# Kernel tuning notes

Hardware: AMD Instinct MI355X
Metric: run time of the kernel (lower is better)

The kernel has to match this reference:

```python
import jax, jax.numpy as jnp
import numpy as np

B, S, D, H = 4, 2048, 1024, 16
DH = D // H


def setup_inputs() -> dict:
    key = jax.random.key(0)
    k1, k2, k3 = jax.random.split(key, 3)
    x = jax.random.normal(k1, (B, S, D), dtype=jnp.float32)
    w_attn = jax.random.normal(k2, (D, 3 * D), dtype=jnp.float32) * 0.02
    b_attn = jnp.zeros((3 * D,), dtype=jnp.float32)
    w_proj = jax.random.normal(k3, (D, D), dtype=jnp.float32) * 0.02
    b_proj = jnp.zeros((D,), dtype=jnp.float32)
    return {"x": x, "w_attn": w_attn, "b_attn": b_attn, "w_proj": w_proj, "b_proj": b_proj}


def _split_heads(t):
    # [B, S, D] -> [B, H, S, DH]
    return t.reshape(B, S, H, DH).transpose(0, 2, 1, 3)


def reference(x, w_attn, b_attn, w_proj, b_proj):
    # fused QKV projection (TFConv1D = x @ w + b)
    qkv = jnp.einsum('bsd,df->bsf', x, w_attn) + b_attn  # [B, S, 3D]
    q, k, v = jnp.split(qkv, 3, axis=2)
    q, k, v = _split_heads(q), _split_heads(k), _split_heads(v)  # [B,H,S,DH]

    # scaled scores
    w = jnp.einsum('bhqd,bhkd->bhqk', q, k) / jnp.sqrt(jnp.asarray(DH, dtype=q.dtype))

    # causal mask: multiply + additive -10000 trick, as in original
    i = jnp.arange(S)[:, None]
    j = jnp.arange(S)[None, :]
    b = (i >= j).astype(w.dtype)  # nd == ns so i >= j - ns + nd == i >= j
    b = b[None, None]  # [1,1,S,S]
    w = w * b - 10000.0 * (1.0 - b)

    w = jax.nn.softmax(w, axis=-1)
    # attn_pdrop = 0.0 -> dropout is identity (eval)

    a = jnp.einsum('bhqk,bhkd->bhqd', w, v)  # [B,H,S,DH]
    a = a.transpose(0, 2, 1, 3).reshape(B, S, D)  # merge heads
    a = jnp.einsum('bsd,df->bsf', a, w_proj) + b_proj
    # resid_pdrop = 0.0 -> identity
    return a
```

## Files before the change

### kernel.cpp

```cpp
#include <hip/hip_runtime.h>
#include <stdint.h>

typedef __bf16 bf16x8 __attribute__((ext_vector_type(8)));
typedef float  f32x4  __attribute__((ext_vector_type(4)));

#define DEV __device__ __forceinline__

constexpr int Bc = 4, S = 2048, D = 1024, Hh = 16, DH = 64;
constexpr int Kdim = 1024;

DEV unsigned short f2bf(float f) {
    uint32_t u = __builtin_bit_cast(uint32_t, f);
    u += 0x7fff + ((u >> 16) & 1);
    return (unsigned short)(u >> 16);
}
DEV bf16x8 ld8(const unsigned short* p) {
    uint4 u = *(const uint4*)p;
    return __builtin_bit_cast(bf16x8, u);
}
DEV uint4 pack8(float4 a, float4 b) {
    union { uint4 u; unsigned short s[8]; } r;
    r.s[0] = f2bf(a.x); r.s[1] = f2bf(a.y); r.s[2] = f2bf(a.z); r.s[3] = f2bf(a.w);
    r.s[4] = f2bf(b.x); r.s[5] = f2bf(b.y); r.s[6] = f2bf(b.z); r.s[7] = f2bf(b.w);
    return r.u;
}

DEV void gl16(const void* g, void* l) {
    __builtin_amdgcn_global_load_lds((__attribute__((address_space(1))) void*)g,
                                     (__attribute__((address_space(3))) void*)l,
                                     16, 0, 0);
}

__global__ __launch_bounds__(256) void transpose_cvt(const float* __restrict__ in,
                                                     unsigned short* __restrict__ out,
                                                     int rows, int cols) {
    __shared__ float t[32][33];
    int tx = threadIdx.x & 31, ty = threadIdx.x >> 5;
    int c = blockIdx.x * 32 + tx;
    int rbase = blockIdx.y * 32;
    for (int rr = 0; rr < 32; rr += 8)
        t[ty + rr][tx] = in[(size_t)(rbase + ty + rr) * cols + c];
    __syncthreads();
    int orbase = blockIdx.x * 32;
    for (int rr = 0; rr < 32; rr += 8)
        out[(size_t)(orbase + ty + rr) * rows + rbase + tx] = f2bf(t[tx][ty + rr]);
}

__global__ __launch_bounds__(256) void cvt_bf16(const float* __restrict__ in,
                                                unsigned short* __restrict__ out) {
    size_t i = (size_t)blockIdx.x * 256 + threadIdx.x;
    const float4* p = (const float4*)(in + i * 8);
    float4 a = p[0], b = p[1];
    *(uint4*)(out + i * 8) = pack8(a, b);
}

__global__ __launch_bounds__(256) void gemm_bt(const unsigned short* __restrict__ A,
                                               const unsigned short* __restrict__ Bt,
                                               const float* __restrict__ bias,
                                               int mode,
                                               unsigned short* __restrict__ qo,
                                               unsigned short* __restrict__ ko,
                                               unsigned short* __restrict__ vo,
                                               float* __restrict__ outf) {
    __shared__ __align__(16) unsigned short As[2][128 * 64];
    __shared__ __align__(16) unsigned short Bs[2][128 * 64];
    const int tid = threadIdx.x;
    const int wave = tid >> 6, lane = tid & 63, g = lane >> 4, ln = lane & 15;
    const int wm = wave >> 1, wn = wave & 1;
    const int nwg = gridDim.x * gridDim.y;
    const int orig = blockIdx.y * gridDim.x + blockIdx.x;
    const int swz = (orig & 7) * (nwg >> 3) + (orig >> 3);
    const int m0 = (swz / gridDim.x) * 128, n0 = (swz % gridDim.x) * 128;

    f32x4 acc[4][4];
    for (int i = 0; i < 4; i++)
        for (int j = 0; j < 4; j++) acc[i][j] = f32x4{0.f, 0.f, 0.f, 0.f};

#define STAGE_G(buf, k0)                                                            \
    _Pragma("unroll")                                                               \
    for (int c = 0; c < 4; c++) {                                                   \
        int L = c * 4096 + tid * 16;                                                \
        int row = L >> 7;                                                           \
        int colb = (L & 127) ^ ((row & 7) << 4);                                    \
        gl16((const char*)A  + ((size_t)(m0 + row) * Kdim + (k0)) * 2 + colb,       \
             (char*)As[buf] + c * 4096 + wave * 1024);                              \
        gl16((const char*)Bt + ((size_t)(n0 + row) * Kdim + (k0)) * 2 + colb,       \
             (char*)Bs[buf] + c * 4096 + wave * 1024);                              \
    }

    STAGE_G(0, 0);
    asm volatile("s_waitcnt vmcnt(0)" ::: "memory");
    __builtin_amdgcn_s_barrier();
    asm volatile("" ::: "memory");

#pragma unroll 1
    for (int t = 0; t < 16; t++) {
        const int buf = t & 1;
        if (t + 1 < 16) STAGE_G(buf ^ 1, (t + 1) * 64);
        const unsigned short* Asb = As[buf];
        const unsigned short* Bsb = Bs[buf];
#pragma unroll
        for (int kk = 0; kk < 2; kk++) {
            bf16x8 af[4], bfr[4];
#pragma unroll
            for (int u = 0; u < 4; u++) {
                int ra = wm * 64 + u * 16 + ln;
                int rb = wn * 64 + u * 16 + ln;
                int co = kk * 64 + g * 16;
                af[u]  = ld8((const unsigned short*)((const char*)Asb + ra * 128 + (co ^ ((ra & 7) << 4))));
                bfr[u] = ld8((const unsigned short*)((const char*)Bsb + rb * 128 + (co ^ ((rb & 7) << 4))));
            }
#pragma unroll
            for (int mt = 0; mt < 4; mt++)
#pragma unroll
                for (int nt = 0; nt < 4; nt++)
                    acc[mt][nt] = __builtin_amdgcn_mfma_f32_16x16x32_bf16(af[mt], bfr[nt], acc[mt][nt], 0, 0, 0);
        }
        asm volatile("" ::: "memory");
        asm volatile("s_waitcnt vmcnt(0)" ::: "memory");
        __builtin_amdgcn_s_barrier();
        asm volatile("" ::: "memory");
    }
#undef STAGE_G

    for (int mt = 0; mt < 4; mt++)
        for (int nt = 0; nt < 4; nt++)
            for (int r = 0; r < 4; r++) {
                int m = m0 + wm * 64 + mt * 16 + g * 4 + r;
                int n = n0 + wn * 64 + nt * 16 + ln;
                float val = acc[mt][nt][r] + bias[n];
                if (mode == 0) {
                    int which = n >> 10, rem = n & 1023;
                    int hh = rem >> 6, dd = rem & 63;
                    int b = m >> 11, s = m & 2047;
                    int bh = (b << 4) + hh;
                    if (which == 0)      qo[((size_t)bh * S + s) * DH + dd] = f2bf(val);
                    else if (which == 1) ko[((size_t)bh * S + s) * DH + dd] = f2bf(val);
                    else                 vo[((size_t)bh * DH + dd) * S + s] = f2bf(val);
                } else {
                    outf[(size_t)m * 1024 + n] = val;
                }
            }
}

__global__ __launch_bounds__(512, 4) void attn_fwd(const unsigned short* __restrict__ qg,
                                                   const unsigned short* __restrict__ kg,
                                                   const unsigned short* __restrict__ vtg,
                                                   unsigned short* __restrict__ og) {
    __shared__ __align__(16) unsigned short Ks[128 * 64];
    __shared__ __align__(16) unsigned short Vs[64 * 128];
    __shared__ __align__(16) unsigned short P [128 * 136];
    const int idx = blockIdx.x;
    const int qt = 15 - (idx >> 6);
    const int bh = idx & 63;
    const int b = bh >> 4, h = bh & 15;
    const size_t base = (size_t)bh * S * DH;
    const unsigned short* qp = qg + base;
    const char* kpb  = (const char*)(kg  + base);
    const char* vtpb = (const char*)(vtg + base);
    const int tid = threadIdx.x, wave = tid >> 6, lane = tid & 63;
    const int g = lane >> 4, ln = lane & 15;
    const int q0 = qt * 128, wq = wave * 16;
    const int jn = qt + 1;

    bf16x8 qf[2];
    qf[0] = ld8(qp + (size_t)(q0 + wq + ln) * DH + g * 8);
    qf[1] = ld8(qp + (size_t)(q0 + wq + ln) * DH + 32 + g * 8);

    f32x4 o_t[4];
#pragma unroll
    for (int dt = 0; dt < 4; dt++) o_t[dt] = f32x4{0.f, 0.f, 0.f, 0.f};
    float m_ = -1e30f, l_ = 0.f;

#pragma unroll 1
    for (int j = 0; j < jn; j++) {
        const char* kj = kpb + (size_t)j * (128 * DH * 2);
        const char* vj = vtpb + j * 256;
#pragma unroll
        for (int c = 0; c < 2; c++) {
            int L = c * 8192 + tid * 16;
            int kr = L >> 7, kcb = L & 127;
            gl16(kj + (size_t)kr * 128 + (kcb ^ ((kr & 7) << 4)),
                 (char*)Ks + c * 8192 + wave * 1024);
            int vr = L >> 8, vcb = L & 255;
            gl16(vj + (size_t)vr * 4096 + (vcb ^ ((vr & 15) << 4)),
                 (char*)Vs + c * 8192 + wave * 1024);
        }
        __syncthreads();

        f32x4 st[8];
#pragma unroll
        for (int mt = 0; mt < 8; mt++) {
            int row = mt * 16 + ln;
            int sw = (row & 7) << 4;
            const char* kb2 = (const char*)Ks + row * 128;
            bf16x8 kf0 = ld8((const unsigned short*)(kb2 + ((g * 16) ^ sw)));
            bf16x8 kf1 = ld8((const unsigned short*)(kb2 + ((64 + g * 16) ^ sw)));
            f32x4 t = f32x4{0.f, 0.f, 0.f, 0.f};
            t = __builtin_amdgcn_mfma_f32_16x16x32_bf16(kf0, qf[0], t, 0, 0, 0);
            t = __builtin_amdgcn_mfma_f32_16x16x32_bf16(kf1, qf[1], t, 0, 0, 0);
            st[mt] = t;
        }
        if (j == jn - 1) {
            int qgl = q0 + wq + ln;
#pragma unroll
            for (int mt = 0; mt < 8; mt++)
#pragma unroll
                for (int r = 0; r < 4; r++) {
                    int kvg = j * 128 + mt * 16 + g * 4 + r;
                    if (kvg > qgl) st[mt][r] = -3e38f;
                }
        }
        f32x4 mm = st[0];
#pragma unroll
        for (int mt = 1; mt < 8; mt++)
#pragma unroll
            for (int e = 0; e < 4; e++) mm[e] = fmaxf(mm[e], st[mt][e]);
        float mx = fmaxf(fmaxf(mm[0], mm[1]), fmaxf(mm[2], mm[3]));
        mx = fmaxf(mx, __shfl_xor(mx, 16));
        mx = fmaxf(mx, __shfl_xor(mx, 32));
        float mnew = fmaxf(m_, mx);
        float alpha = __expf((m_ - mnew) * 0.125f);
        f32x4 sv = f32x4{0.f, 0.f, 0.f, 0.f};
#pragma unroll
        for (int mt = 0; mt < 8; mt++) {
            f32x4 pr;
#pragma unroll
            for (int e = 0; e < 4; e++) pr[e] = __expf((st[mt][e] - mnew) * 0.125f);
            st[mt] = pr;
            sv += pr;
        }
        float rs = (sv[0] + sv[1]) + (sv[2] + sv[3]);
        rs += __shfl_xor(rs, 16);
        rs += __shfl_xor(rs, 32);
        l_ = l_ * alpha + rs;
        m_ = mnew;

#pragma unroll
        for (int mt = 0; mt < 8; mt++) {
            uint4 u = __builtin_bit_cast(uint4, st[mt]);
            uint2 w;
            w.x = (u.y & 0xFFFF0000u) | (u.x >> 16);
            w.y = (u.w & 0xFFFF0000u) | (u.z >> 16);
            *(uint2*)&P[(wq + ln) * 136 + mt * 16 + g * 4] = w;
        }
#pragma unroll
        for (int dt = 0; dt < 4; dt++) o_t[dt] *= alpha;

#pragma unroll
        for (int kc = 0; kc < 4; kc++) {
            bf16x8 pf = ld8(&P[(wq + ln) * 136 + kc * 32 + g * 8]);
            bf16x8 vf[4];
#pragma unroll
            for (int dt = 0; dt < 4; dt++) {
                int row = dt * 16 + ln;
                vf[dt] = ld8((const unsigned short*)((const char*)Vs + row * 256 +
                             ((kc * 64 + g * 16) ^ ((row & 15) << 4))));
            }
#pragma unroll
            for (int dt = 0; dt < 4; dt++)
                o_t[dt] = __builtin_amdgcn_mfma_f32_16x16x32_bf16(vf[dt], pf, o_t[dt], 0, 0, 0);
        }
        __syncthreads();
    }

    float il = 1.f / l_;
#pragma unroll
    for (int dt = 0; dt < 4; dt++) o_t[dt] *= il;
    float* Ot = (float*)&P[wq * 136];
#pragma unroll
    for (int dt = 0; dt < 4; dt++)
        *(float4*)&Ot[ln * 68 + dt * 16 + g * 4] =
            float4{o_t[dt][0], o_t[dt][1], o_t[dt][2], o_t[dt][3]};
#pragma unroll
    for (int i = 0; i < 4; i++) {
        float4 v = *(float4*)&Ot[(i * 4 + g) * 68 + ln * 4];
        uint2 w;
        w.x = (uint32_t)f2bf(v.x) | ((uint32_t)f2bf(v.y) << 16);
        w.y = (uint32_t)f2bf(v.z) | ((uint32_t)f2bf(v.w) << 16);
        *(uint2*)&og[((size_t)(b * S + q0 + wq + i * 4 + g)) * D + h * DH + ln * 4] = w;
    }
}

extern "C" void kernel_launch(void* const* d_in, const int* in_sizes, int n_in,
                              void* d_out, int out_size, void* d_ws, size_t ws_size,
                              hipStream_t stream) {
    (void)in_sizes; (void)n_in; (void)out_size; (void)ws_size;
    const float* x      = (const float*)d_in[0];
    const float* w_attn = (const float*)d_in[1];
    const float* b_attn = (const float*)d_in[2];
    const float* w_proj = (const float*)d_in[3];
    const float* b_proj = (const float*)d_in[4];

    char* ws = (char*)d_ws;
    unsigned short* wattn_t = (unsigned short*)ws;
    unsigned short* wproj_t = (unsigned short*)(ws + 6291456);
    unsigned short* xb      = (unsigned short*)(ws + 8388608);
    unsigned short* qb      = (unsigned short*)(ws + 25165824);
    unsigned short* kb      = (unsigned short*)(ws + 41943040);
    unsigned short* vtb     = (unsigned short*)(ws + 58720256);
    unsigned short* aob     = (unsigned short*)(ws + 75497472);

    transpose_cvt<<<dim3(96, 32), 256, 0, stream>>>(w_attn, wattn_t, 1024, 3072);
    transpose_cvt<<<dim3(32, 32), 256, 0, stream>>>(w_proj, wproj_t, 1024, 1024);
    cvt_bf16<<<dim3(4096), 256, 0, stream>>>(x, xb);
    gemm_bt<<<dim3(24, 64), 256, 0, stream>>>(xb, wattn_t, b_attn, 0, qb, kb, vtb, nullptr);
    attn_fwd<<<dim3(1024), 512, 0, stream>>>(qb, kb, vtb, aob);
    gemm_bt<<<dim3(8, 64), 256, 0, stream>>>(aob, wproj_t, b_proj, 1,
                                             nullptr, nullptr, nullptr, (float*)d_out);
}
```

Before: 264.5 us.

## Triple-buffer GEMM K-loop and software-pipeline K/V loads in attention

The GEMM now uses a three-stage LDS ring with 32-wide K slices, keeping two tiles of global loads in flight with partial vmcnt waits instead of draining every iteration. The attention kernel is restructured so the PV product of the previous block runs while the next K tile and the current V tile are loading, with the final PV step peeled after the loop. The aim is to hide global-to-LDS latency behind MFMA work. In exchange there are more barriers per K step, a more complex index mapping, and subtle ordering hazards around the reuse of the shared K/V/P buffers.

```diff
diff --git a/kernel.cpp b/kernel.cpp
--- a/kernel.cpp
+++ b/kernel.cpp
@@ -62,8 +62,8 @@
                                                unsigned short* __restrict__ ko,
                                                unsigned short* __restrict__ vo,
                                                float* __restrict__ outf) {
-    __shared__ __align__(16) unsigned short As[2][128 * 64];
-    __shared__ __align__(16) unsigned short Bs[2][128 * 64];
+    __shared__ __align__(16) unsigned short As[3][4096];
+    __shared__ __align__(16) unsigned short Bs[3][4096];
     const int tid = threadIdx.x;
     const int wave = tid >> 6, lane = tid & 63, g = lane >> 4, ln = lane & 15;
     const int wm = wave >> 1, wn = wave & 1;
@@ -78,46 +78,46 @@
 
 #define STAGE_G(buf, k0)                                                            \
     _Pragma("unroll")                                                               \
-    for (int c = 0; c < 4; c++) {                                                   \
+    for (int c = 0; c < 2; c++) {                                                   \
         int L = c * 4096 + tid * 16;                                                \
-        int row = L >> 7;                                                           \
-        int colb = (L & 127) ^ ((row & 7) << 4);                                    \
-        gl16((const char*)A  + ((size_t)(m0 + row) * Kdim + (k0)) * 2 + colb,       \
+        int lr = L >> 7;                                                            \
+        int bp = (L & 127) ^ ((lr & 7) << 4);                                       \
+        int rr = lr * 2 + (bp >> 6), cb = bp & 63;                                  \
+        gl16((const char*)A  + ((size_t)(m0 + rr) * Kdim + (k0)) * 2 + cb,          \
              (char*)As[buf] + c * 4096 + wave * 1024);                              \
-        gl16((const char*)Bt + ((size_t)(n0 + row) * Kdim + (k0)) * 2 + colb,       \
+        gl16((const char*)Bt + ((size_t)(n0 + rr) * Kdim + (k0)) * 2 + cb,          \
              (char*)Bs[buf] + c * 4096 + wave * 1024);                              \
     }
 
     STAGE_G(0, 0);
-    asm volatile("s_waitcnt vmcnt(0)" ::: "memory");
+    STAGE_G(1, 32);
+    asm volatile("s_waitcnt vmcnt(4)" ::: "memory");
     __builtin_amdgcn_s_barrier();
     asm volatile("" ::: "memory");
 
 #pragma unroll 1
-    for (int t = 0; t < 16; t++) {
-        const int buf = t & 1;
-        if (t + 1 < 16) STAGE_G(buf ^ 1, (t + 1) * 64);
+    for (int t = 0; t < 32; t++) {
+        const int buf = t % 3;
+        if (t + 2 < 32) { STAGE_G((t + 2) % 3, (t + 2) * 32); }
         const unsigned short* Asb = As[buf];
         const unsigned short* Bsb = Bs[buf];
-#pragma unroll
-        for (int kk = 0; kk < 2; kk++) {
-            bf16x8 af[4], bfr[4];
-#pragma unroll
-            for (int u = 0; u < 4; u++) {
-                int ra = wm * 64 + u * 16 + ln;
-                int rb = wn * 64 + u * 16 + ln;
-                int co = kk * 64 + g * 16;
-                af[u]  = ld8((const unsigned short*)((const char*)Asb + ra * 128 + (co ^ ((ra & 7) << 4))));
-                bfr[u] = ld8((const unsigned short*)((const char*)Bsb + rb * 128 + (co ^ ((rb & 7) << 4))));
-            }
-#pragma unroll
-            for (int mt = 0; mt < 4; mt++)
-#pragma unroll
-                for (int nt = 0; nt < 4; nt++)
-                    acc[mt][nt] = __builtin_amdgcn_mfma_f32_16x16x32_bf16(af[mt], bfr[nt], acc[mt][nt], 0, 0, 0);
-        }
+        bf16x8 af[4], bfr[4];
+#pragma unroll
+        for (int u = 0; u < 4; u++) {
+            int lra = wm * 32 + u * 8 + (ln >> 1);
+            int lrb = wn * 32 + u * 8 + (ln >> 1);
+            int bb  = ((ln & 1) << 6) | (g << 4);
+            af[u]  = ld8((const unsigned short*)((const char*)Asb + lra * 128 + (bb ^ ((lra & 7) << 4))));
+            bfr[u] = ld8((const unsigned short*)((const char*)Bsb + lrb * 128 + (bb ^ ((lrb & 7) << 4))));
+        }
+#pragma unroll
+        for (int mt = 0; mt < 4; mt++)
+#pragma unroll
+            for (int nt = 0; nt < 4; nt++)
+                acc[mt][nt] = __builtin_amdgcn_mfma_f32_16x16x32_bf16(af[mt], bfr[nt], acc[mt][nt], 0, 0, 0);
         asm volatile("" ::: "memory");
-        asm volatile("s_waitcnt vmcnt(0)" ::: "memory");
+        if (t < 30) asm volatile("s_waitcnt vmcnt(4)" ::: "memory");
+        else        asm volatile("s_waitcnt vmcnt(0)" ::: "memory");
         __builtin_amdgcn_s_barrier();
         asm volatile("" ::: "memory");
     }
@@ -167,6 +167,32 @@
     qf[0] = ld8(qp + (size_t)(q0 + wq + ln) * DH + g * 8);
     qf[1] = ld8(qp + (size_t)(q0 + wq + ln) * DH + 32 + g * 8);
 
+#define STAGE_K(j)                                                                  \
+    {   const char* kj = kpb + (size_t)(j) * (128 * DH * 2);                        \
+        _Pragma("unroll")                                                           \
+        for (int c = 0; c < 2; c++) {                                               \
+            int L = c * 8192 + tid * 16;                                            \
+            int kr = L >> 7, kcb = L & 127;                                         \
+            gl16(kj + (size_t)kr * 128 + (kcb ^ ((kr & 7) << 4)),                   \
+                 (char*)Ks + c * 8192 + wave * 1024);                               \
+        }                                                                           \
+    }
+#define STAGE_V(j)                                                                  \
+    {   const char* vj = vtpb + (j) * 256;                                          \
+        _Pragma("unroll")                                                           \
+        for (int c = 0; c < 2; c++) {                                               \
+            int L = c * 8192 + tid * 16;                                            \
+            int vr = L >> 8, vcb = L & 255;                                         \
+            gl16(vj + (size_t)vr * 4096 + (vcb ^ ((vr & 15) << 4)),                 \
+                 (char*)Vs + c * 8192 + wave * 1024);                               \
+        }                                                                           \
+    }
+
+    STAGE_K(0);
+    asm volatile("s_waitcnt vmcnt(0)" ::: "memory");
+    __builtin_amdgcn_s_barrier();
+    asm volatile("" ::: "memory");
+
     f32x4 o_t[4];
 #pragma unroll
     for (int dt = 0; dt < 4; dt++) o_t[dt] = f32x4{0.f, 0.f, 0.f, 0.f};
@@ -174,20 +200,6 @@
 
 #pragma unroll 1
     for (int j = 0; j < jn; j++) {
-        const char* kj = kpb + (size_t)j * (128 * DH * 2);
-        const char* vj = vtpb + j * 256;
-#pragma unroll
-        for (int c = 0; c < 2; c++) {
-            int L = c * 8192 + tid * 16;
-            int kr = L >> 7, kcb = L & 127;
-            gl16(kj + (size_t)kr * 128 + (kcb ^ ((kr & 7) << 4)),
-                 (char*)Ks + c * 8192 + wave * 1024);
-            int vr = L >> 8, vcb = L & 255;
-            gl16(vj + (size_t)vr * 4096 + (vcb ^ ((vr & 15) << 4)),
-                 (char*)Vs + c * 8192 + wave * 1024);
-        }
-        __syncthreads();
-
         f32x4 st[8];
 #pragma unroll
         for (int mt = 0; mt < 8; mt++) {
@@ -201,6 +213,27 @@
             t = __builtin_amdgcn_mfma_f32_16x16x32_bf16(kf1, qf[1], t, 0, 0, 0);
             st[mt] = t;
         }
+        if (j > 0) {
+#pragma unroll
+            for (int kc = 0; kc < 4; kc++) {
+                bf16x8 pf = ld8(&P[(wq + ln) * 136 + kc * 32 + g * 8]);
+                bf16x8 vf[4];
+#pragma unroll
+                for (int dt = 0; dt < 4; dt++) {
+                    int row = dt * 16 + ln;
+                    vf[dt] = ld8((const unsigned short*)((const char*)Vs + row * 256 +
+                                 ((kc * 64 + g * 16) ^ ((row & 15) << 4))));
+                }
+#pragma unroll
+                for (int dt = 0; dt < 4; dt++)
+                    o_t[dt] = __builtin_amdgcn_mfma_f32_16x16x32_bf16(vf[dt], pf, o_t[dt], 0, 0, 0);
+            }
+        }
+        __builtin_amdgcn_s_barrier();
+        asm volatile("" ::: "memory");
+        if (j + 1 < jn) STAGE_K(j + 1);
+        STAGE_V(j);
+
         if (j == jn - 1) {
             int qgl = q0 + wq + ln;
 #pragma unroll
@@ -247,21 +280,26 @@
 #pragma unroll
         for (int dt = 0; dt < 4; dt++) o_t[dt] *= alpha;
 
-#pragma unroll
-        for (int kc = 0; kc < 4; kc++) {
-            bf16x8 pf = ld8(&P[(wq + ln) * 136 + kc * 32 + g * 8]);
-            bf16x8 vf[4];
-#pragma unroll
-            for (int dt = 0; dt < 4; dt++) {
-                int row = dt * 16 + ln;
-                vf[dt] = ld8((const unsigned short*)((const char*)Vs + row * 256 +
-                             ((kc * 64 + g * 16) ^ ((row & 15) << 4))));
-            }
-#pragma unroll
-            for (int dt = 0; dt < 4; dt++)
-                o_t[dt] = __builtin_amdgcn_mfma_f32_16x16x32_bf16(vf[dt], pf, o_t[dt], 0, 0, 0);
-        }
-        __syncthreads();
+        asm volatile("s_waitcnt vmcnt(0)" ::: "memory");
+        __builtin_amdgcn_s_barrier();
+        asm volatile("" ::: "memory");
+    }
+#undef STAGE_K
+#undef STAGE_V
+
+#pragma unroll
+    for (int kc = 0; kc < 4; kc++) {
+        bf16x8 pf = ld8(&P[(wq + ln) * 136 + kc * 32 + g * 8]);
+        bf16x8 vf[4];
+#pragma unroll
+        for (int dt = 0; dt < 4; dt++) {
+            int row = dt * 16 + ln;
+            vf[dt] = ld8((const unsigned short*)((const char*)Vs + row * 256 +
+                         ((kc * 64 + g * 16) ^ ((row & 15) << 4))));
+        }
+#pragma unroll
+        for (int dt = 0; dt < 4; dt++)
+            o_t[dt] = __builtin_amdgcn_mfma_f32_16x16x32_bf16(vf[dt], pf, o_t[dt], 0, 0, 0);
     }
 
     float il = 1.f / l_;
```

Measured after the change: 275.9 us. +4.3%, slower.

## Double-buffer K/V tiles, widen per-wave query rows, pair causal tiles per block

Applied to the files above, without the earlier changes.

The attention kernel now processes 256 query rows per block, with each wave handling 32 rows so every K/V fragment read from LDS feeds two MFMA chains. K/V tiles are double-buffered in shared memory, so the next tile's global loads are issued while the current one is computed, using a single barrier per iteration. Each block handles a long and a short causal query tile (7-pair and pair) to balance work across a grid of 256 blocks. This costs more registers and LDS, occupancy drops to launch bounds of 2, and there are fewer blocks than before, which risks underfilling the CUs.

```diff
diff --git a/kernel.cpp b/kernel.cpp
--- a/kernel.cpp
+++ b/kernel.cpp
@@ -143,143 +143,198 @@
             }
 }
 
-__global__ __launch_bounds__(512, 4) void attn_fwd(const unsigned short* __restrict__ qg,
+__global__ __launch_bounds__(512, 2) void attn_fwd(const unsigned short* __restrict__ qg,
                                                    const unsigned short* __restrict__ kg,
                                                    const unsigned short* __restrict__ vtg,
                                                    unsigned short* __restrict__ og) {
-    __shared__ __align__(16) unsigned short Ks[128 * 64];
-    __shared__ __align__(16) unsigned short Vs[64 * 128];
-    __shared__ __align__(16) unsigned short P [128 * 136];
+    __shared__ __align__(16) unsigned short Ks[2][128 * 64];
+    __shared__ __align__(16) unsigned short Vs[2][64 * 128];
+    __shared__ __align__(16) unsigned short P [256 * 136];
     const int idx = blockIdx.x;
-    const int qt = 15 - (idx >> 6);
+    const int pair = idx >> 6;
     const int bh = idx & 63;
-    const int b = bh >> 4, h = bh & 15;
+    const int b = bh >> 4, hd = bh & 15;
     const size_t base = (size_t)bh * S * DH;
     const unsigned short* qp = qg + base;
     const char* kpb  = (const char*)(kg  + base);
     const char* vtpb = (const char*)(vtg + base);
     const int tid = threadIdx.x, wave = tid >> 6, lane = tid & 63;
     const int g = lane >> 4, ln = lane & 15;
-    const int q0 = qt * 128, wq = wave * 16;
-    const int jn = qt + 1;
-
-    bf16x8 qf[2];
-    qf[0] = ld8(qp + (size_t)(q0 + wq + ln) * DH + g * 8);
-    qf[1] = ld8(qp + (size_t)(q0 + wq + ln) * DH + 32 + g * 8);
-
-    f32x4 o_t[4];
-#pragma unroll
-    for (int dt = 0; dt < 4; dt++) o_t[dt] = f32x4{0.f, 0.f, 0.f, 0.f};
-    float m_ = -1e30f, l_ = 0.f;
+    const int wq = wave * 32;
+
+#define STAGE_K(j, bf)                                                              \
+    {   const char* kj = kpb + (size_t)(j) * (128 * DH * 2);                        \
+        _Pragma("unroll")                                                           \
+        for (int c = 0; c < 2; c++) {                                               \
+            int L = c * 8192 + tid * 16;                                            \
+            int kr = L >> 7, kcb = L & 127;                                         \
+            gl16(kj + (size_t)kr * 128 + (kcb ^ ((kr & 7) << 4)),                   \
+                 (char*)Ks[bf] + c * 8192 + wave * 1024);                           \
+        }                                                                           \
+    }
+#define STAGE_V(j, bf)                                                              \
+    {   const char* vj = vtpb + (j) * 256;                                          \
+        _Pragma("unroll")                                                           \
+        for (int c = 0; c < 2; c++) {                                               \
+            int L = c * 8192 + tid * 16;                                            \
+            int vr = L >> 8, vcb = L & 255;                                         \
+            gl16(vj + (size_t)vr * 4096 + (vcb ^ ((vr & 15) << 4)),                 \
+                 (char*)Vs[bf] + c * 8192 + wave * 1024);                           \
+        }                                                                           \
+    }
 
 #pragma unroll 1
-    for (int j = 0; j < jn; j++) {
-        const char* kj = kpb + (size_t)j * (128 * DH * 2);
-        const char* vj = vtpb + j * 256;
-#pragma unroll
-        for (int c = 0; c < 2; c++) {
-            int L = c * 8192 + tid * 16;
-            int kr = L >> 7, kcb = L & 127;
-            gl16(kj + (size_t)kr * 128 + (kcb ^ ((kr & 7) << 4)),
-                 (char*)Ks + c * 8192 + wave * 1024);
-            int vr = L >> 8, vcb = L & 255;
-            gl16(vj + (size_t)vr * 4096 + (vcb ^ ((vr & 15) << 4)),
-                 (char*)Vs + c * 8192 + wave * 1024);
+    for (int t2 = 0; t2 < 2; t2++) {
+        const int qt = t2 ? pair : (7 - pair);
+        const int q0 = qt * 256;
+        const int jn = 2 * qt + 2;
+
+        bf16x8 qf[2][2];
+#pragma unroll
+        for (int h = 0; h < 2; h++)
+#pragma unroll
+            for (int c = 0; c < 2; c++)
+                qf[h][c] = ld8(qp + (size_t)(q0 + wq + h * 16 + ln) * DH + c * 32 + g * 8);
+
+        STAGE_K(0, 0);
+        STAGE_V(0, 0);
+        asm volatile("s_waitcnt vmcnt(0)" ::: "memory");
+        __builtin_amdgcn_s_barrier();
+        asm volatile("" ::: "memory");
+
+        f32x4 o_t[4][2];
+#pragma unroll
+        for (int dt = 0; dt < 4; dt++)
+#pragma unroll
+            for (int h = 0; h < 2; h++) o_t[dt][h] = f32x4{0.f, 0.f, 0.f, 0.f};
+        float m_[2] = {-1e30f, -1e30f}, l_[2] = {0.f, 0.f};
+
+#pragma unroll 1
+        for (int j = 0; j < jn; j++) {
+            const int buf = j & 1;
+            if (j + 1 < jn) { STAGE_K(j + 1, buf ^ 1); STAGE_V(j + 1, buf ^ 1); }
+
+            f32x4 st[8][2];
+#pragma unroll
+            for (int mt = 0; mt < 8; mt++) {
+                int row = mt * 16 + ln;
+                int sw = (row & 7) << 4;
+                const char* kb2 = (const char*)Ks[buf] + row * 128;
+                bf16x8 kf0 = ld8((const unsigned short*)(kb2 + ((g * 16) ^ sw)));
+                bf16x8 kf1 = ld8((const unsigned short*)(kb2 + ((64 + g * 16) ^ sw)));
+#pragma unroll
+                for (int h = 0; h < 2; h++) {
+                    f32x4 t = f32x4{0.f, 0.f, 0.f, 0.f};
+                    t = __builtin_amdgcn_mfma_f32_16x16x32_bf16(kf0, qf[h][0], t, 0, 0, 0);
+                    t = __builtin_amdgcn_mfma_f32_16x16x32_bf16(kf1, qf[h][1], t, 0, 0, 0);
+                    st[mt][h] = t;
+                }
+            }
+            if (j >= jn - 2) {
+#pragma unroll
+                for (int h = 0; h < 2; h++) {
+                    int qgl = q0 + wq + h * 16 + ln;
+#pragma unroll
+                    for (int mt = 0; mt < 8; mt++)
+#pragma unroll
+                        for (int r = 0; r < 4; r++) {
+                            int kvg = j * 128 + mt * 16 + g * 4 + r;
+                            if (kvg > qgl) st[mt][h][r] = -3e38f;
+                        }
+                }
+            }
+            float alpha[2];
+#pragma unroll
+            for (int h = 0; h < 2; h++) {
+                f32x4 mm = st[0][h];
+#pragma unroll
+                for (int mt = 1; mt < 8; mt++)
+#pragma unroll
+                    for (int e = 0; e < 4; e++) mm[e] = fmaxf(mm[e], st[mt][h][e]);
+                float mx = fmaxf(fmaxf(mm[0], mm[1]), fmaxf(mm[2], mm[3]));
+                mx = fmaxf(mx, __shfl_xor(mx, 16));
+                mx = fmaxf(mx, __shfl_xor(mx, 32));
+                float mnew = fmaxf(m_[h], mx);
+                alpha[h] = __expf((m_[h] - mnew) * 0.125f);
+                f32x4 sv = f32x4{0.f, 0.f, 0.f, 0.f};
+#pragma unroll
+                for (int mt = 0; mt < 8; mt++) {
+                    f32x4 pr;
+#pragma unroll
+                    for (int e = 0; e < 4; e++) pr[e] = __expf((st[mt][h][e] - mnew) * 0.125f);
+                    st[mt][h] = pr;
+                    sv += pr;
+                }
+                float rs = (sv[0] + sv[1]) + (sv[2] + sv[3]);
+                rs += __shfl_xor(rs, 16);
+                rs += __shfl_xor(rs, 32);
+                l_[h] = l_[h] * alpha[h] + rs;
+                m_[h] = mnew;
+            }
+#pragma unroll
+            for (int h = 0; h < 2; h++)
+#pragma unroll
+                for (int mt = 0; mt < 8; mt++) {
+                    uint4 u = __builtin_bit_cast(uint4, st[mt][h]);
+                    uint2 w;
+                    w.x = (u.y & 0xFFFF0000u) | (u.x >> 16);
+                    w.y = (u.w & 0xFFFF0000u) | (u.z >> 16);
+                    *(uint2*)&P[(wq + h * 16 + ln) * 136 + mt * 16 + g * 4] = w;
+                }
+#pragma unroll
+            for (int dt = 0; dt < 4; dt++)
+#pragma unroll
+                for (int h = 0; h < 2; h++) o_t[dt][h] *= alpha[h];
+
+#pragma unroll
+            for (int kc = 0; kc < 4; kc++) {
+                bf16x8 pf[2];
+#pragma unroll
+                for (int h = 0; h < 2; h++)
+                    pf[h] = ld8(&P[(wq + h * 16 + ln) * 136 + kc * 32 + g * 8]);
+                bf16x8 vf[4];
+#pragma unroll
+                for (int dt = 0; dt < 4; dt++) {
+                    int row = dt * 16 + ln;
+                    vf[dt] = ld8((const unsigned short*)((const char*)Vs[buf] + row * 256 +
+                                 ((kc * 64 + g * 16) ^ ((row & 15) << 4))));
+                }
+#pragma unroll
+                for (int dt = 0; dt < 4; dt++)
+#pragma unroll
+                    for (int h = 0; h < 2; h++)
+                        o_t[dt][h] = __builtin_amdgcn_mfma_f32_16x16x32_bf16(vf[dt], pf[h], o_t[dt][h], 0, 0, 0);
+            }
+            asm volatile("" ::: "memory");
+            if (j + 1 < jn) asm volatile("s_waitcnt vmcnt(0)" ::: "memory");
+            __builtin_amdgcn_s_barrier();
+            asm volatile("" ::: "memory");
         }
-        __syncthreads();
-
-        f32x4 st[8];
-#pragma unroll
-        for (int mt = 0; mt < 8; mt++) {
-            int row = mt * 16 + ln;
-            int sw = (row & 7) << 4;
-            const char* kb2 = (const char*)Ks + row * 128;
-            bf16x8 kf0 = ld8((const unsigned short*)(kb2 + ((g * 16) ^ sw)));
-            bf16x8 kf1 = ld8((const unsigned short*)(kb2 + ((64 + g * 16) ^ sw)));
-            f32x4 t = f32x4{0.f, 0.f, 0.f, 0.f};
-            t = __builtin_amdgcn_mfma_f32_16x16x32_bf16(kf0, qf[0], t, 0, 0, 0);
-            t = __builtin_amdgcn_mfma_f32_16x16x32_bf16(kf1, qf[1], t, 0, 0, 0);
-            st[mt] = t;
+
+#pragma unroll
+        for (int h = 0; h < 2; h++) {
+            float il = 1.f / l_[h];
+#pragma unroll
+            for (int dt = 0; dt < 4; dt++) o_t[dt][h] *= il;
         }
-        if (j == jn - 1) {
-            int qgl = q0 + wq + ln;
-#pragma unroll
-            for (int mt = 0; mt < 8; mt++)
-#pragma unroll
-                for (int r = 0; r < 4; r++) {
-                    int kvg = j * 128 + mt * 16 + g * 4 + r;
-                    if (kvg > qgl) st[mt][r] = -3e38f;
-                }
+        float* Ot = (float*)&P[wq * 136];
+#pragma unroll
+        for (int h = 0; h < 2; h++)
+#pragma unroll
+            for (int dt = 0; dt < 4; dt++)
+                *(float4*)&Ot[(h * 16 + ln) * 68 + dt * 16 + g * 4] =
+                    float4{o_t[dt][h][0], o_t[dt][h][1], o_t[dt][h][2], o_t[dt][h][3]};
+#pragma unroll
+        for (int i = 0; i < 8; i++) {
+            float4 v = *(float4*)&Ot[(i * 4 + g) * 68 + ln * 4];
+            uint2 w;
+            w.x = (uint32_t)f2bf(v.x) | ((uint32_t)f2bf(v.y) << 16);
+            w.y = (uint32_t)f2bf(v.z) | ((uint32_t)f2bf(v.w) << 16);
+            *(uint2*)&og[((size_t)(b * S + q0 + wq + i * 4 + g)) * D + hd * DH + ln * 4] = w;
         }
-        f32x4 mm = st[0];
-#pragma unroll
-        for (int mt = 1; mt < 8; mt++)
-#pragma unroll
-            for (int e = 0; e < 4; e++) mm[e] = fmaxf(mm[e], st[mt][e]);
-        float mx = fmaxf(fmaxf(mm[0], mm[1]), fmaxf(mm[2], mm[3]));
-        mx = fmaxf(mx, __shfl_xor(mx, 16));
-        mx = fmaxf(mx, __shfl_xor(mx, 32));
-        float mnew = fmaxf(m_, mx);
-        float alpha = __expf((m_ - mnew) * 0.125f);
-        f32x4 sv = f32x4{0.f, 0.f, 0.f, 0.f};
-#pragma unroll
-        for (int mt = 0; mt < 8; mt++) {
-            f32x4 pr;
-#pragma unroll
-            for (int e = 0; e < 4; e++) pr[e] = __expf((st[mt][e] - mnew) * 0.125f);
-            st[mt] = pr;
-            sv += pr;
-        }
-        float rs = (sv[0] + sv[1]) + (sv[2] + sv[3]);
-        rs += __shfl_xor(rs, 16);
-        rs += __shfl_xor(rs, 32);
-        l_ = l_ * alpha + rs;
-        m_ = mnew;
-
-#pragma unroll
-        for (int mt = 0; mt < 8; mt++) {
-            uint4 u = __builtin_bit_cast(uint4, st[mt]);
-            uint2 w;
-            w.x = (u.y & 0xFFFF0000u) | (u.x >> 16);
-            w.y = (u.w & 0xFFFF0000u) | (u.z >> 16);
-            *(uint2*)&P[(wq + ln) * 136 + mt * 16 + g * 4] = w;
-        }
-#pragma unroll
-        for (int dt = 0; dt < 4; dt++) o_t[dt] *= alpha;
-
-#pragma unroll
-        for (int kc = 0; kc < 4; kc++) {
-            bf16x8 pf = ld8(&P[(wq + ln) * 136 + kc * 32 + g * 8]);
-            bf16x8 vf[4];
-#pragma unroll
-            for (int dt = 0; dt < 4; dt++) {
-                int row = dt * 16 + ln;
-                vf[dt] = ld8((const unsigned short*)((const char*)Vs + row * 256 +
-                             ((kc * 64 + g * 16) ^ ((row & 15) << 4))));
-            }
-#pragma unroll
-            for (int dt = 0; dt < 4; dt++)
-                o_t[dt] = __builtin_amdgcn_mfma_f32_16x16x32_bf16(vf[dt], pf, o_t[dt], 0, 0, 0);
-        }
-        __syncthreads();
-    }
-
-    float il = 1.f / l_;
-#pragma unroll
-    for (int dt = 0; dt < 4; dt++) o_t[dt] *= il;
-    float* Ot = (float*)&P[wq * 136];
-#pragma unroll
-    for (int dt = 0; dt < 4; dt++)
-        *(float4*)&Ot[ln * 68 + dt * 16 + g * 4] =
-            float4{o_t[dt][0], o_t[dt][1], o_t[dt][2], o_t[dt][3]};
-#pragma unroll
-    for (int i = 0; i < 4; i++) {
-        float4 v = *(float4*)&Ot[(i * 4 + g) * 68 + ln * 4];
-        uint2 w;
-        w.x = (uint32_t)f2bf(v.x) | ((uint32_t)f2bf(v.y) << 16);
-        w.y = (uint32_t)f2bf(v.z) | ((uint32_t)f2bf(v.w) << 16);
-        *(uint2*)&og[((size_t)(b * S + q0 + wq + i * 4 + g)) * D + h * DH + ln * 4] = w;
-    }
+    }
+#undef STAGE_K
+#undef STAGE_V
 }
 
 extern "C" void kernel_launch(void* const* d_in, const int* in_sizes, int n_in,
@@ -305,7 +360,7 @@
     transpose_cvt<<<dim3(32, 32), 256, 0, stream>>>(w_proj, wproj_t, 1024, 1024);
     cvt_bf16<<<dim3(4096), 256, 0, stream>>>(x, xb);
     gemm_bt<<<dim3(24, 64), 256, 0, stream>>>(xb, wattn_t, b_attn, 0, qb, kb, vtb, nullptr);
-    attn_fwd<<<dim3(1024), 512, 0, stream>>>(qb, kb, vtb, aob);
+    attn_fwd<<<dim3(256), 512, 0, stream>>>(qb, kb, vtb, aob);
     gemm_bt<<<dim3(8, 64), 256, 0, stream>>>(aob, wproj_t, b_proj, 1,
                                              nullptr, nullptr, nullptr, (float*)d_out);
 }
```

After: 273.0 us. 3.2% more time.

## Double-buffer K/V tiles, use 256-row query blocks, pair causal tiles per block

Applied to the files above, without the earlier changes.

Attention now runs 1024-thread blocks covering 256 query rows. Each block processes two query tiles (pair and 7-pair) so causal work is balanced across blocks. K/V tiles are double-buffered in shared memory, and the next tile is prefetched while the current one computes, with raw barriers and vmcnt waits replacing __syncthreads. MFMA sections are wrapped in s_setprio. The aim is to hide global load latency and even out the causal triangle, at the cost of more LDS per block, lower occupancy, and only 256 blocks in the grid.

```diff
diff --git a/kernel.cpp b/kernel.cpp
--- a/kernel.cpp
+++ b/kernel.cpp
@@ -143,143 +143,168 @@
             }
 }
 
-__global__ __launch_bounds__(512, 4) void attn_fwd(const unsigned short* __restrict__ qg,
-                                                   const unsigned short* __restrict__ kg,
-                                                   const unsigned short* __restrict__ vtg,
-                                                   unsigned short* __restrict__ og) {
-    __shared__ __align__(16) unsigned short Ks[128 * 64];
-    __shared__ __align__(16) unsigned short Vs[64 * 128];
-    __shared__ __align__(16) unsigned short P [128 * 136];
+__global__ __launch_bounds__(1024, 4) void attn_fwd(const unsigned short* __restrict__ qg,
+                                                    const unsigned short* __restrict__ kg,
+                                                    const unsigned short* __restrict__ vtg,
+                                                    unsigned short* __restrict__ og) {
+    __shared__ __align__(16) unsigned short Ks[2][128 * 64];
+    __shared__ __align__(16) unsigned short Vs[2][64 * 128];
+    __shared__ __align__(16) unsigned short P [256 * 136];
     const int idx = blockIdx.x;
-    const int qt = 15 - (idx >> 6);
+    const int pair = idx >> 6;
     const int bh = idx & 63;
-    const int b = bh >> 4, h = bh & 15;
+    const int b = bh >> 4, hd = bh & 15;
     const size_t base = (size_t)bh * S * DH;
     const unsigned short* qp = qg + base;
     const char* kpb  = (const char*)(kg  + base);
     const char* vtpb = (const char*)(vtg + base);
     const int tid = threadIdx.x, wave = tid >> 6, lane = tid & 63;
     const int g = lane >> 4, ln = lane & 15;
-    const int q0 = qt * 128, wq = wave * 16;
-    const int jn = qt + 1;
-
-    bf16x8 qf[2];
-    qf[0] = ld8(qp + (size_t)(q0 + wq + ln) * DH + g * 8);
-    qf[1] = ld8(qp + (size_t)(q0 + wq + ln) * DH + 32 + g * 8);
-
-    f32x4 o_t[4];
-#pragma unroll
-    for (int dt = 0; dt < 4; dt++) o_t[dt] = f32x4{0.f, 0.f, 0.f, 0.f};
-    float m_ = -1e30f, l_ = 0.f;
+    const int wq = wave * 16;
+
+#define STAGE_K(j, bf)                                                              \
+    {   const char* kj = kpb + (size_t)(j) * (128 * DH * 2);                        \
+        int L = tid * 16;                                                           \
+        int kr = L >> 7, kcb = L & 127;                                             \
+        gl16(kj + (size_t)kr * 128 + (kcb ^ ((kr & 7) << 4)),                       \
+             (char*)Ks[bf] + wave * 1024);                                          \
+    }
+#define STAGE_V(j, bf)                                                              \
+    {   const char* vj = vtpb + (j) * 256;                                          \
+        int L = tid * 16;                                                           \
+        int vr = L >> 8, vcb = L & 255;                                             \
+        gl16(vj + (size_t)vr * 4096 + (vcb ^ ((vr & 15) << 4)),                     \
+             (char*)Vs[bf] + wave * 1024);                                          \
+    }
 
 #pragma unroll 1
-    for (int j = 0; j < jn; j++) {
-        const char* kj = kpb + (size_t)j * (128 * DH * 2);
-        const char* vj = vtpb + j * 256;
-#pragma unroll
-        for (int c = 0; c < 2; c++) {
-            int L = c * 8192 + tid * 16;
-            int kr = L >> 7, kcb = L & 127;
-            gl16(kj + (size_t)kr * 128 + (kcb ^ ((kr & 7) << 4)),
-                 (char*)Ks + c * 8192 + wave * 1024);
-            int vr = L >> 8, vcb = L & 255;
-            gl16(vj + (size_t)vr * 4096 + (vcb ^ ((vr & 15) << 4)),
-                 (char*)Vs + c * 8192 + wave * 1024);
+    for (int t2 = 0; t2 < 2; t2++) {
+        const int qt = t2 ? pair : (7 - pair);
+        const int q0 = qt * 256;
+        const int jn = 2 * qt + 2;
+
+        bf16x8 qf[2];
+        qf[0] = ld8(qp + (size_t)(q0 + wq + ln) * DH + g * 8);
+        qf[1] = ld8(qp + (size_t)(q0 + wq + ln) * DH + 32 + g * 8);
+
+        STAGE_K(0, 0);
+        STAGE_V(0, 0);
+        asm volatile("s_waitcnt vmcnt(0)" ::: "memory");
+        __builtin_amdgcn_s_barrier();
+        asm volatile("" ::: "memory");
+
+        f32x4 o_t[4];
+#pragma unroll
+        for (int dt = 0; dt < 4; dt++) o_t[dt] = f32x4{0.f, 0.f, 0.f, 0.f};
+        float m_ = -1e30f, l_ = 0.f;
+
+#pragma unroll 1
+        for (int j = 0; j < jn; j++) {
+            const int buf = j & 1;
+            if (j + 1 < jn) { STAGE_K(j + 1, buf ^ 1); STAGE_V(j + 1, buf ^ 1); }
+
+            f32x4 st[8];
+            __builtin_amdgcn_s_setprio(1);
+#pragma unroll
+            for (int mt = 0; mt < 8; mt++) {
+                int row = mt * 16 + ln;
+                int sw = (row & 7) << 4;
+                const char* kb2 = (const char*)Ks[buf] + row * 128;
+                bf16x8 kf0 = ld8((const unsigned short*)(kb2 + ((g * 16) ^ sw)));
+                bf16x8 kf1 = ld8((const unsigned short*)(kb2 + ((64 + g * 16) ^ sw)));
+                f32x4 t = f32x4{0.f, 0.f, 0.f, 0.f};
+                t = __builtin_amdgcn_mfma_f32_16x16x32_bf16(kf0, qf[0], t, 0, 0, 0);
+                t = __builtin_amdgcn_mfma_f32_16x16x32_bf16(kf1, qf[1], t, 0, 0, 0);
+                st[mt] = t;
+            }
+            __builtin_amdgcn_s_setprio(0);
+            if (j >= jn - 2) {
+                int qgl = q0 + wq + ln;
+#pragma unroll
+                for (int mt = 0; mt < 8; mt++)
+#pragma unroll
+                    for (int r = 0; r < 4; r++) {
+                        int kvg = j * 128 + mt * 16 + g * 4 + r;
+                        if (kvg > qgl) st[mt][r] = -3e38f;
+                    }
+            }
+            f32x4 mm = st[0];
+#pragma unroll
+            for (int mt = 1; mt < 8; mt++)
+#pragma unroll
+                for (int e = 0; e < 4; e++) mm[e] = fmaxf(mm[e], st[mt][e]);
+            float mx = fmaxf(fmaxf(mm[0], mm[1]), fmaxf(mm[2], mm[3]));
+            mx = fmaxf(mx, __shfl_xor(mx, 16));
+            mx = fmaxf(mx, __shfl_xor(mx, 32));
+            float mnew = fmaxf(m_, mx);
+            float alpha = __expf((m_ - mnew) * 0.125f);
+            f32x4 sv = f32x4{0.f, 0.f, 0.f, 0.f};
+#pragma unroll
+            for (int mt = 0; mt < 8; mt++) {
+                f32x4 pr;
+#pragma unroll
+                for (int e = 0; e < 4; e++) pr[e] = __expf((st[mt][e] - mnew) * 0.125f);
+                st[mt] = pr;
+                sv += pr;
+            }
+            float rs = (sv[0] + sv[1]) + (sv[2] + sv[3]);
+            rs += __shfl_xor(rs, 16);
+            rs += __shfl_xor(rs, 32);
+            l_ = l_ * alpha + rs;
+            m_ = mnew;
+
+#pragma unroll
+            for (int mt = 0; mt < 8; mt++) {
+                uint4 u = __builtin_bit_cast(uint4, st[mt]);
+                uint2 w;
+                w.x = (u.y & 0xFFFF0000u) | (u.x >> 16);
+                w.y = (u.w & 0xFFFF0000u) | (u.z >> 16);
+                *(uint2*)&P[(wq + ln) * 136 + mt * 16 + g * 4] = w;
+            }
+#pragma unroll
+            for (int dt = 0; dt < 4; dt++) o_t[dt] *= alpha;
+
+            __builtin_amdgcn_s_setprio(1);
+#pragma unroll
+            for (int kc = 0; kc < 4; kc++) {
+                bf16x8 pf = ld8(&P[(wq + ln) * 136 + kc * 32 + g * 8]);
+                bf16x8 vf[4];
+#pragma unroll
+                for (int dt = 0; dt < 4; dt++) {
+                    int row = dt * 16 + ln;
+                    vf[dt] = ld8((const unsigned short*)((const char*)Vs[buf] + row * 256 +
+                                 ((kc * 64 + g * 16) ^ ((row & 15) << 4))));
+                }
+#pragma unroll
+                for (int dt = 0; dt < 4; dt++)
+                    o_t[dt] = __builtin_amdgcn_mfma_f32_16x16x32_bf16(vf[dt], pf, o_t[dt], 0, 0, 0);
+            }
+            __builtin_amdgcn_s_setprio(0);
+            asm volatile("" ::: "memory");
+            if (j + 1 < jn) asm volatile("s_waitcnt vmcnt(0)" ::: "memory");
+            __builtin_amdgcn_s_barrier();
+            asm volatile("" ::: "memory");
         }
-        __syncthreads();
-
-        f32x4 st[8];
-#pragma unroll
-        for (int mt = 0; mt < 8; mt++) {
-            int row = mt * 16 + ln;
-            int sw = (row & 7) << 4;
-            const char* kb2 = (const char*)Ks + row * 128;
-            bf16x8 kf0 = ld8((const unsigned short*)(kb2 + ((g * 16) ^ sw)));
-            bf16x8 kf1 = ld8((const unsigned short*)(kb2 + ((64 + g * 16) ^ sw)));
-            f32x4 t = f32x4{0.f, 0.f, 0.f, 0.f};
-            t = __builtin_amdgcn_mfma_f32_16x16x32_bf16(kf0, qf[0], t, 0, 0, 0);
-            t = __builtin_amdgcn_mfma_f32_16x16x32_bf16(kf1, qf[1], t, 0, 0, 0);
-            st[mt] = t;
+
+        float il = 1.f / l_;
+#pragma unroll
+        for (int dt = 0; dt < 4; dt++) o_t[dt] *= il;
+        float* Ot = (float*)&P[wq * 136];
+#pragma unroll
+        for (int dt = 0; dt < 4; dt++)
+            *(float4*)&Ot[ln * 68 + dt * 16 + g * 4] =
+                float4{o_t[dt][0], o_t[dt][1], o_t[dt][2], o_t[dt][3]};
+#pragma unroll
+        for (int i = 0; i < 4; i++) {
+            float4 v = *(float4*)&Ot[(i * 4 + g) * 68 + ln * 4];
+            uint2 w;
+            w.x = (uint32_t)f2bf(v.x) | ((uint32_t)f2bf(v.y) << 16);
+            w.y = (uint32_t)f2bf(v.z) | ((uint32_t)f2bf(v.w) << 16);
+            *(uint2*)&og[((size_t)(b * S + q0 + wq + i * 4 + g)) * D + hd * DH + ln * 4] = w;
         }
-        if (j == jn - 1) {
-            int qgl = q0 + wq + ln;
-#pragma unroll
-            for (int mt = 0; mt < 8; mt++)
-#pragma unroll
-                for (int r = 0; r < 4; r++) {
-                    int kvg = j * 128 + mt * 16 + g * 4 + r;
-                    if (kvg > qgl) st[mt][r] = -3e38f;
-                }
-        }
-        f32x4 mm = st[0];
-#pragma unroll
-        for (int mt = 1; mt < 8; mt++)
-#pragma unroll
-            for (int e = 0; e < 4; e++) mm[e] = fmaxf(mm[e], st[mt][e]);
-        float mx = fmaxf(fmaxf(mm[0], mm[1]), fmaxf(mm[2], mm[3]));
-        mx = fmaxf(mx, __shfl_xor(mx, 16));
-        mx = fmaxf(mx, __shfl_xor(mx, 32));
-        float mnew = fmaxf(m_, mx);
-        float alpha = __expf((m_ - mnew) * 0.125f);
-        f32x4 sv = f32x4{0.f, 0.f, 0.f, 0.f};
-#pragma unroll
-        for (int mt = 0; mt < 8; mt++) {
-            f32x4 pr;
-#pragma unroll
-            for (int e = 0; e < 4; e++) pr[e] = __expf((st[mt][e] - mnew) * 0.125f);
-            st[mt] = pr;
-            sv += pr;
-        }
-        float rs = (sv[0] + sv[1]) + (sv[2] + sv[3]);
-        rs += __shfl_xor(rs, 16);
-        rs += __shfl_xor(rs, 32);
-        l_ = l_ * alpha + rs;
-        m_ = mnew;
-
-#pragma unroll
-        for (int mt = 0; mt < 8; mt++) {
-            uint4 u = __builtin_bit_cast(uint4, st[mt]);
-            uint2 w;
-            w.x = (u.y & 0xFFFF0000u) | (u.x >> 16);
-            w.y = (u.w & 0xFFFF0000u) | (u.z >> 16);
-            *(uint2*)&P[(wq + ln) * 136 + mt * 16 + g * 4] = w;
-        }
-#pragma unroll
-        for (int dt = 0; dt < 4; dt++) o_t[dt] *= alpha;
-
-#pragma unroll
-        for (int kc = 0; kc < 4; kc++) {
-            bf16x8 pf = ld8(&P[(wq + ln) * 136 + kc * 32 + g * 8]);
-            bf16x8 vf[4];
-#pragma unroll
-            for (int dt = 0; dt < 4; dt++) {
-                int row = dt * 16 + ln;
-                vf[dt] = ld8((const unsigned short*)((const char*)Vs + row * 256 +
-                             ((kc * 64 + g * 16) ^ ((row & 15) << 4))));
-            }
-#pragma unroll
-            for (int dt = 0; dt < 4; dt++)
-                o_t[dt] = __builtin_amdgcn_mfma_f32_16x16x32_bf16(vf[dt], pf, o_t[dt], 0, 0, 0);
-        }
-        __syncthreads();
-    }
-
-    float il = 1.f / l_;
-#pragma unroll
-    for (int dt = 0; dt < 4; dt++) o_t[dt] *= il;
-    float* Ot = (float*)&P[wq * 136];
-#pragma unroll
-    for (int dt = 0; dt < 4; dt++)
-        *(float4*)&Ot[ln * 68 + dt * 16 + g * 4] =
-            float4{o_t[dt][0], o_t[dt][1], o_t[dt][2], o_t[dt][3]};
-#pragma unroll
-    for (int i = 0; i < 4; i++) {
-        float4 v = *(float4*)&Ot[(i * 4 + g) * 68 + ln * 4];
-        uint2 w;
-        w.x = (uint32_t)f2bf(v.x) | ((uint32_t)f2bf(v.y) << 16);
-        w.y = (uint32_t)f2bf(v.z) | ((uint32_t)f2bf(v.w) << 16);
-        *(uint2*)&og[((size_t)(b * S + q0 + wq + i * 4 + g)) * D + h * DH + ln * 4] = w;
-    }
+    }
+#undef STAGE_K
+#undef STAGE_V
 }
 
 extern "C" void kernel_launch(void* const* d_in, const int* in_sizes, int n_in,
@@ -305,7 +330,7 @@
     transpose_cvt<<<dim3(32, 32), 256, 0, stream>>>(w_proj, wproj_t, 1024, 1024);
     cvt_bf16<<<dim3(4096), 256, 0, stream>>>(x, xb);
     gemm_bt<<<dim3(24, 64), 256, 0, stream>>>(xb, wattn_t, b_attn, 0, qb, kb, vtb, nullptr);
-    attn_fwd<<<dim3(1024), 512, 0, stream>>>(qb, kb, vtb, aob);
+    attn_fwd<<<dim3(256), 1024, 0, stream>>>(qb, kb, vtb, aob);
     gemm_bt<<<dim3(8, 64), 256, 0, stream>>>(aob, wproj_t, b_proj, 1,
                                              nullptr, nullptr, nullptr, (float*)d_out);
 }
```

Result: no change. 266.8 us (+0.8%).
